# Performance work log

Measured on AMD Instinct MI355X. Metric: run time of the kernel, lower is better.

Reference implementation:

```python
import jax, jax.numpy as jnp
import numpy as np

N_NODES = 50000
N_EDGES = 800000
D = 128
# PNA avg_deg['log'] from deg histogram: all 50000 nodes have degree 16
# avg_deg_log = sum(log(i+1)*deg[i]) / sum(deg) = log(17)
AVG_DEG_LOG = float(np.log(17.0))
EPS = 1e-5  # PyG StdAggregation epsilon


def setup_inputs() -> dict:
    key = jax.random.key(0)
    k1, k2, k3 = jax.random.split(key, 3)
    x = jax.random.normal(k1, (N_EDGES, D), jnp.float32)
    index = jax.random.randint(k2, (N_EDGES,), 0, N_NODES)
    # nn.Linear(12*D, D): weight [out, in]
    W = jax.random.normal(k3, (D, 12 * D), jnp.float32) * 0.02
    b = jnp.zeros((D,), jnp.float32)
    return {"x": x, "index": index, "W": W, "b": b}


def reference(x, index, W, b):
    N = N_NODES
    ones = jnp.ones((x.shape[0],), x.dtype)
    cnt = jax.ops.segment_sum(ones, index, num_segments=N)          # [N] degree
    cnt_c = jnp.maximum(cnt, 1.0)[:, None]                          # clamp(1)
    s1 = jax.ops.segment_sum(x, index, num_segments=N)              # [N, D]
    s2 = jax.ops.segment_sum(x * x, index, num_segments=N)          # [N, D]
    mean = s1 / cnt_c
    var = s2 / cnt_c - mean * mean
    std = jnp.sqrt(jax.nn.relu(var) + EPS)
    mn = jax.ops.segment_min(x, index, num_segments=N)
    mx = jax.ops.segment_max(x, index, num_segments=N)
    empty = (cnt == 0.0)[:, None]
    mn = jnp.where(empty, 0.0, mn)  # torch_scatter fills empty segments with 0
    mx = jnp.where(empty, 0.0, mx)
    agg = jnp.concatenate([mean, mn, mx, std], axis=-1)             # [N, 4D]
    logd = jnp.log(jnp.maximum(cnt, 1.0) + 1.0)[:, None]
    amp = agg * (logd / AVG_DEG_LOG)                                # amplification
    att = agg * (AVG_DEG_LOG / logd)                                # attenuation
    out = jnp.concatenate([agg, amp, att], axis=-1)                 # [N, 12D]
    return out @ W.T + b                                            # [N, D]
```

## Files before the change

kernel.cpp:

```cpp
#include <hip/hip_runtime.h>
#include <hip/hip_bf16.h>

typedef __attribute__((ext_vector_type(8))) __bf16 bf16x8;
typedef __attribute__((ext_vector_type(4))) float f32x4;

#define AVG_DEG_LOG 2.833213344056216f

__device__ __forceinline__ unsigned short f2bf(float f) {
  union { float f; unsigned int u; } a; a.f = f;
  unsigned int r = a.u + 0x7FFFu + ((a.u >> 16) & 1u);
  return (unsigned short)(r >> 16);
}

__global__ void hist_kernel(const int* __restrict__ idx, int* __restrict__ cnt, int E) {
  int i = blockIdx.x * blockDim.x + threadIdx.x;
  if (i < E) atomicAdd(&cnt[idx[i]], 1);
}

__global__ __launch_bounds__(1024) void scan_kernel(const int* __restrict__ cnt,
                                                    int* __restrict__ offsets, int N) {
  __shared__ int partial[1024];
  int t = threadIdx.x;
  int CH = (N + 1023) >> 10;
  int base = t * CH;
  int s = 0;
  for (int i = 0; i < CH; ++i) { int id = base + i; if (id < N) s += cnt[id]; }
  partial[t] = s;
  __syncthreads();
  int val = s;
  for (int off = 1; off < 1024; off <<= 1) {
    int add = (t >= off) ? partial[t - off] : 0;
    __syncthreads();
    val += add;
    partial[t] = val;
    __syncthreads();
  }
  int run = val - s;
  for (int i = 0; i < CH; ++i) {
    int id = base + i;
    if (id < N) { offsets[id] = run; run += cnt[id]; }
  }
  if (t == 1023) offsets[N] = run;
}

__global__ void scatter_kernel(const int* __restrict__ idx, const int* __restrict__ offsets,
                               int* __restrict__ cursor, int* __restrict__ edge_ids, int E) {
  int i = blockIdx.x * blockDim.x + threadIdx.x;
  if (i < E) {
    int n = idx[i];
    int p = atomicAdd(&cursor[n], 1);
    edge_ids[offsets[n] + p] = i;
  }
}

__global__ void wconv_kernel(const float* __restrict__ W, unsigned short* __restrict__ Wb, int n4) {
  int i = blockIdx.x * blockDim.x + threadIdx.x;
  if (i < n4) {
    float4 v = ((const float4*)W)[i];
    ushort4 o;
    o.x = f2bf(v.x); o.y = f2bf(v.y); o.z = f2bf(v.z); o.w = f2bf(v.w);
    ((ushort4*)Wb)[i] = o;
  }
}

__global__ __launch_bounds__(256) void agg_kernel(const float* __restrict__ x,
    const int* __restrict__ edge_ids, const int* __restrict__ offsets,
    unsigned short* __restrict__ agg4, float* __restrict__ amp, float* __restrict__ att, int Nn) {
  int wid = blockIdx.x * 4 + (threadIdx.x >> 6);
  if (wid >= Nn) return;
  int lane = threadIdx.x & 63;
  int offs = offsets[wid];
  int deg = offsets[wid + 1] - offs;
  float s0 = 0.f, s1 = 0.f, q0 = 0.f, q1 = 0.f;
  float mn0 = INFINITY, mn1 = INFINITY, mx0 = -INFINITY, mx1 = -INFINITY;
  int f0 = lane * 2;
  for (int i = 0; i < deg; i += 64) {
    int myid = 0;
    if (i + lane < deg) myid = edge_ids[offs + i + lane];
    int c = deg - i; if (c > 64) c = 64;
    for (int ii = 0; ii < c; ++ii) {
      int e = __shfl(myid, ii, 64);
      float2 v = *(const float2*)(x + (size_t)e * 128 + f0);
      s0 += v.x; s1 += v.y;
      q0 += v.x * v.x; q1 += v.y * v.y;
      mn0 = fminf(mn0, v.x); mn1 = fminf(mn1, v.y);
      mx0 = fmaxf(mx0, v.x); mx1 = fmaxf(mx1, v.y);
    }
  }
  float c = deg > 0 ? (float)deg : 1.0f;
  float inv = 1.0f / c;
  float m0 = s0 * inv, m1 = s1 * inv;
  float v0 = q0 * inv - m0 * m0; v0 = v0 > 0.f ? v0 : 0.f;
  float v1 = q1 * inv - m1 * m1; v1 = v1 > 0.f ? v1 : 0.f;
  float sd0 = sqrtf(v0 + 1e-5f), sd1 = sqrtf(v1 + 1e-5f);
  if (deg == 0) { mn0 = mn1 = mx0 = mx1 = 0.f; }
  size_t rb = (size_t)wid * 512;
  ((unsigned int*)(agg4 + rb      ))[lane] = (unsigned)f2bf(m0)  | ((unsigned)f2bf(m1)  << 16);
  ((unsigned int*)(agg4 + rb + 128))[lane] = (unsigned)f2bf(mn0) | ((unsigned)f2bf(mn1) << 16);
  ((unsigned int*)(agg4 + rb + 256))[lane] = (unsigned)f2bf(mx0) | ((unsigned)f2bf(mx1) << 16);
  ((unsigned int*)(agg4 + rb + 384))[lane] = (unsigned)f2bf(sd0) | ((unsigned)f2bf(sd1) << 16);
  if (lane == 0) {
    float ld = logf(c + 1.0f);
    amp[wid] = ld / AVG_DEG_LOG;
    att[wid] = AVG_DEG_LOG / ld;
  }
}

__global__ __launch_bounds__(256) void gemm_kernel(
    const unsigned short* __restrict__ agg4, const unsigned short* __restrict__ Wb,
    const float* __restrict__ amp, const float* __restrict__ att,
    const float* __restrict__ bias, float* __restrict__ out, int Nn) {
  __shared__ __align__(16) unsigned short As[64][40];
  __shared__ __align__(16) unsigned short Bs[3][128][40];
  __shared__ float ampS[64], attS[64];
  int t = threadIdx.x;
  int m0 = blockIdx.x * 64;
  if (t < 64) {
    int n = m0 + t; if (n > Nn - 1) n = Nn - 1;
    ampS[t] = amp[n]; attS[t] = att[n];
  }
  int wave = t >> 6, lane = t & 63;
  int arow = lane & 15, quad = lane >> 4;
  f32x4 acc[3][8];
#pragma unroll
  for (int g = 0; g < 3; ++g)
#pragma unroll
    for (int c8 = 0; c8 < 8; ++c8) acc[g][c8] = (f32x4){0.f, 0.f, 0.f, 0.f};

  int ar = t >> 2;
  int akc = (t & 3) * 8;
  int agr = m0 + ar; if (agr > Nn - 1) agr = Nn - 1;
  const unsigned short* aptr = agg4 + (size_t)agr * 512 + akc;

  for (int kk = 0; kk < 512; kk += 32) {
    __syncthreads();
    *(uint4*)&As[ar][akc] = *(const uint4*)(aptr + kk);
#pragma unroll
    for (int j = 0; j < 6; ++j) {
      int idx = t + j * 256;
      int g = idx >> 9;
      int rem = idx & 511;
      int n = rem >> 2;
      int kc = (rem & 3) * 8;
      *(uint4*)&Bs[g][n][kc] = *(const uint4*)(Wb + (size_t)n * 1536 + g * 512 + kk + kc);
    }
    __syncthreads();
    bf16x8 af = *(bf16x8*)&As[wave * 16 + arow][quad * 8];
#pragma unroll
    for (int g = 0; g < 3; ++g) {
#pragma unroll
      for (int c8 = 0; c8 < 8; ++c8) {
        bf16x8 bf = *(bf16x8*)&Bs[g][c8 * 16 + arow][quad * 8];
        acc[g][c8] = __builtin_amdgcn_mfma_f32_16x16x32_bf16(af, bf, acc[g][c8], 0, 0, 0);
      }
    }
  }
#pragma unroll
  for (int c8 = 0; c8 < 8; ++c8) {
    int col = c8 * 16 + arow;
    float bv = bias[col];
#pragma unroll
    for (int r = 0; r < 4; ++r) {
      int lrow = wave * 16 + quad * 4 + r;
      int n = m0 + lrow;
      if (n < Nn) {
        float o = acc[0][c8][r] + ampS[lrow] * acc[1][c8][r] + attS[lrow] * acc[2][c8][r] + bv;
        out[(size_t)n * 128 + col] = o;
      }
    }
  }
}

extern "C" void kernel_launch(void* const* d_in, const int* in_sizes, int n_in,
                              void* d_out, int out_size, void* d_ws, size_t ws_size,
                              hipStream_t stream) {
  const float* x     = (const float*)d_in[0];
  const int*   index = (const int*)d_in[1];
  const float* W     = (const float*)d_in[2];
  const float* bias  = (const float*)d_in[3];
  int E  = in_sizes[1];
  int Nn = out_size / 128;
  float* out = (float*)d_out;

  char* ws = (char*)d_ws;
  size_t off = 0;
  int* cnt     = (int*)(ws + off); off += (size_t)Nn * 4;
  int* cursor  = (int*)(ws + off); off += (size_t)Nn * 4;
  int* offsets = (int*)(ws + off); off += (size_t)(Nn + 1) * 4;
  off = (off + 255) & ~(size_t)255;
  int* edge_ids = (int*)(ws + off); off += (size_t)E * 4;
  off = (off + 255) & ~(size_t)255;
  unsigned short* agg4 = (unsigned short*)(ws + off); off += (size_t)Nn * 512 * 2;
  float* amp = (float*)(ws + off); off += (size_t)Nn * 4;
  float* att = (float*)(ws + off); off += (size_t)Nn * 4;
  off = (off + 255) & ~(size_t)255;
  unsigned short* Wb = (unsigned short*)(ws + off); off += (size_t)128 * 1536 * 2;

  hipMemsetAsync(ws, 0, (size_t)Nn * 8, stream);

  int eb = (E + 255) / 256;
  hist_kernel<<<eb, 256, 0, stream>>>(index, cnt, E);
  scan_kernel<<<1, 1024, 0, stream>>>(cnt, offsets, Nn);
  scatter_kernel<<<eb, 256, 0, stream>>>(index, offsets, cursor, edge_ids, E);
  int n4 = 128 * 1536 / 4;
  wconv_kernel<<<(n4 + 255) / 256, 256, 0, stream>>>(W, Wb, n4);
  agg_kernel<<<(Nn + 3) / 4, 256, 0, stream>>>(x, edge_ids, offsets, agg4, amp, att, Nn);
  gemm_kernel<<<(Nn + 63) / 64, 256, 0, stream>>>(agg4, Wb, amp, att, bias, out, Nn);
}
```

Before: 796.6 us.

## Widen agg gathers to float4 with half-wave edge split and fuse hist/wconv

The aggregation kernel now has each half-wave handle a different edge. Each lane loads a 16-byte float4 slice of a row instead of 8 bytes. The gather loop is unrolled to keep four independent non-temporal loads in flight, and the two halves' partials are combined with a cross-half shuffle. The histogram and weight-conversion kernels are merged into one launch to remove a launch. This aims to raise memory-level parallelism on the dominant random-row gather, at the cost of more registers, a remainder path and a final shuffle reduction.

```diff
diff --git a/kernel.cpp b/kernel.cpp
--- a/kernel.cpp
+++ b/kernel.cpp
@@ -12,9 +12,29 @@
   return (unsigned short)(r >> 16);
 }
 
-__global__ void hist_kernel(const int* __restrict__ idx, int* __restrict__ cnt, int E) {
-  int i = blockIdx.x * blockDim.x + threadIdx.x;
-  if (i < E) atomicAdd(&cnt[idx[i]], 1);
+__device__ __forceinline__ uint2 pack4(f32x4 a) {
+  uint2 u;
+  u.x = (unsigned)f2bf(a[0]) | ((unsigned)f2bf(a[1]) << 16);
+  u.y = (unsigned)f2bf(a[2]) | ((unsigned)f2bf(a[3]) << 16);
+  return u;
+}
+
+__global__ void hist_wconv_kernel(const int* __restrict__ idx, int* __restrict__ cnt, int E,
+                                  int hb, const float* __restrict__ W,
+                                  unsigned short* __restrict__ Wb, int n4) {
+  int b = blockIdx.x;
+  if (b < hb) {
+    int i = b * 256 + threadIdx.x;
+    if (i < E) atomicAdd(&cnt[idx[i]], 1);
+  } else {
+    int i = (b - hb) * 256 + threadIdx.x;
+    if (i < n4) {
+      float4 v = ((const float4*)W)[i];
+      ushort4 o;
+      o.x = f2bf(v.x); o.y = f2bf(v.y); o.z = f2bf(v.z); o.w = f2bf(v.w);
+      ((ushort4*)Wb)[i] = o;
+    }
+  }
 }
 
 __global__ __launch_bounds__(1024) void scan_kernel(const int* __restrict__ cnt,
@@ -53,54 +73,86 @@
   }
 }
 
-__global__ void wconv_kernel(const float* __restrict__ W, unsigned short* __restrict__ Wb, int n4) {
-  int i = blockIdx.x * blockDim.x + threadIdx.x;
-  if (i < n4) {
-    float4 v = ((const float4*)W)[i];
-    ushort4 o;
-    o.x = f2bf(v.x); o.y = f2bf(v.y); o.z = f2bf(v.z); o.w = f2bf(v.w);
-    ((ushort4*)Wb)[i] = o;
-  }
-}
-
 __global__ __launch_bounds__(256) void agg_kernel(const float* __restrict__ x,
     const int* __restrict__ edge_ids, const int* __restrict__ offsets,
     unsigned short* __restrict__ agg4, float* __restrict__ amp, float* __restrict__ att, int Nn) {
   int wid = blockIdx.x * 4 + (threadIdx.x >> 6);
   if (wid >= Nn) return;
   int lane = threadIdx.x & 63;
+  int half = lane >> 5;
+  int fh = (lane & 31) * 4;
   int offs = offsets[wid];
   int deg = offsets[wid + 1] - offs;
-  float s0 = 0.f, s1 = 0.f, q0 = 0.f, q1 = 0.f;
-  float mn0 = INFINITY, mn1 = INFINITY, mx0 = -INFINITY, mx1 = -INFINITY;
-  int f0 = lane * 2;
+  f32x4 s = {0.f, 0.f, 0.f, 0.f}, q = {0.f, 0.f, 0.f, 0.f};
+  f32x4 mn = {INFINITY, INFINITY, INFINITY, INFINITY};
+  f32x4 mx = {-INFINITY, -INFINITY, -INFINITY, -INFINITY};
+  const float* xb = x + fh;
   for (int i = 0; i < deg; i += 64) {
     int myid = 0;
     if (i + lane < deg) myid = edge_ids[offs + i + lane];
     int c = deg - i; if (c > 64) c = 64;
-    for (int ii = 0; ii < c; ++ii) {
-      int e = __shfl(myid, ii, 64);
-      float2 v = *(const float2*)(x + (size_t)e * 128 + f0);
-      s0 += v.x; s1 += v.y;
-      q0 += v.x * v.x; q1 += v.y * v.y;
-      mn0 = fminf(mn0, v.x); mn1 = fminf(mn1, v.y);
-      mx0 = fmaxf(mx0, v.x); mx1 = fmaxf(mx1, v.y);
-    }
-  }
-  float c = deg > 0 ? (float)deg : 1.0f;
-  float inv = 1.0f / c;
-  float m0 = s0 * inv, m1 = s1 * inv;
-  float v0 = q0 * inv - m0 * m0; v0 = v0 > 0.f ? v0 : 0.f;
-  float v1 = q1 * inv - m1 * m1; v1 = v1 > 0.f ? v1 : 0.f;
-  float sd0 = sqrtf(v0 + 1e-5f), sd1 = sqrtf(v1 + 1e-5f);
-  if (deg == 0) { mn0 = mn1 = mx0 = mx1 = 0.f; }
+    int ii = 0;
+    for (; ii + 8 <= c; ii += 8) {
+      int e0 = __shfl(myid, ii + half, 64);
+      int e1 = __shfl(myid, ii + 2 + half, 64);
+      int e2 = __shfl(myid, ii + 4 + half, 64);
+      int e3 = __shfl(myid, ii + 6 + half, 64);
+      f32x4 v0 = __builtin_nontemporal_load((const f32x4*)(xb + (size_t)e0 * 128));
+      f32x4 v1 = __builtin_nontemporal_load((const f32x4*)(xb + (size_t)e1 * 128));
+      f32x4 v2 = __builtin_nontemporal_load((const f32x4*)(xb + (size_t)e2 * 128));
+      f32x4 v3 = __builtin_nontemporal_load((const f32x4*)(xb + (size_t)e3 * 128));
+#pragma unroll
+      for (int j = 0; j < 4; ++j) {
+        s[j] += v0[j]; q[j] += v0[j] * v0[j]; mn[j] = fminf(mn[j], v0[j]); mx[j] = fmaxf(mx[j], v0[j]);
+        s[j] += v1[j]; q[j] += v1[j] * v1[j]; mn[j] = fminf(mn[j], v1[j]); mx[j] = fmaxf(mx[j], v1[j]);
+        s[j] += v2[j]; q[j] += v2[j] * v2[j]; mn[j] = fminf(mn[j], v2[j]); mx[j] = fmaxf(mx[j], v2[j]);
+        s[j] += v3[j]; q[j] += v3[j] * v3[j]; mn[j] = fminf(mn[j], v3[j]); mx[j] = fmaxf(mx[j], v3[j]);
+      }
+    }
+    for (; ii < c; ii += 2) {
+      int p = ii + half;
+      bool valid = p < c;
+      int e = __shfl(myid, valid ? p : c - 1, 64);
+      f32x4 v = __builtin_nontemporal_load((const f32x4*)(xb + (size_t)e * 128));
+      if (valid) {
+#pragma unroll
+        for (int j = 0; j < 4; ++j) {
+          s[j] += v[j]; q[j] += v[j] * v[j]; mn[j] = fminf(mn[j], v[j]); mx[j] = fmaxf(mx[j], v[j]);
+        }
+      }
+    }
+  }
+#pragma unroll
+  for (int j = 0; j < 4; ++j) {
+    s[j] += __shfl_xor(s[j], 32, 64);
+    q[j] += __shfl_xor(q[j], 32, 64);
+    mn[j] = fminf(mn[j], __shfl_xor(mn[j], 32, 64));
+    mx[j] = fmaxf(mx[j], __shfl_xor(mx[j], 32, 64));
+  }
+  float cdeg = deg > 0 ? (float)deg : 1.0f;
+  float inv = 1.0f / cdeg;
+  f32x4 mean, sd;
+#pragma unroll
+  for (int j = 0; j < 4; ++j) {
+    mean[j] = s[j] * inv;
+    float var = q[j] * inv - mean[j] * mean[j];
+    var = var > 0.f ? var : 0.f;
+    sd[j] = sqrtf(var + 1e-5f);
+  }
+  if (deg == 0) {
+#pragma unroll
+    for (int j = 0; j < 4; ++j) { mn[j] = 0.f; mx[j] = 0.f; }
+  }
   size_t rb = (size_t)wid * 512;
-  ((unsigned int*)(agg4 + rb      ))[lane] = (unsigned)f2bf(m0)  | ((unsigned)f2bf(m1)  << 16);
-  ((unsigned int*)(agg4 + rb + 128))[lane] = (unsigned)f2bf(mn0) | ((unsigned)f2bf(mn1) << 16);
-  ((unsigned int*)(agg4 + rb + 256))[lane] = (unsigned)f2bf(mx0) | ((unsigned)f2bf(mx1) << 16);
-  ((unsigned int*)(agg4 + rb + 384))[lane] = (unsigned)f2bf(sd0) | ((unsigned)f2bf(sd1) << 16);
+  if (half == 0) {
+    *(uint2*)(agg4 + rb + fh)       = pack4(mean);
+    *(uint2*)(agg4 + rb + 128 + fh) = pack4(mn);
+  } else {
+    *(uint2*)(agg4 + rb + 256 + fh) = pack4(mx);
+    *(uint2*)(agg4 + rb + 384 + fh) = pack4(sd);
+  }
   if (lane == 0) {
-    float ld = logf(c + 1.0f);
+    float ld = logf(cdeg + 1.0f);
     amp[wid] = ld / AVG_DEG_LOG;
     att[wid] = AVG_DEG_LOG / ld;
   }
@@ -199,11 +251,11 @@
   hipMemsetAsync(ws, 0, (size_t)Nn * 8, stream);
 
   int eb = (E + 255) / 256;
-  hist_kernel<<<eb, 256, 0, stream>>>(index, cnt, E);
+  int n4 = 128 * 1536 / 4;
+  int wb = (n4 + 255) / 256;
+  hist_wconv_kernel<<<eb + wb, 256, 0, stream>>>(index, cnt, E, eb, W, Wb, n4);
   scan_kernel<<<1, 1024, 0, stream>>>(cnt, offsets, Nn);
   scatter_kernel<<<eb, 256, 0, stream>>>(index, offsets, cursor, edge_ids, E);
-  int n4 = 128 * 1536 / 4;
-  wconv_kernel<<<(n4 + 255) / 256, 256, 0, stream>>>(W, Wb, n4);
   agg_kernel<<<(Nn + 3) / 4, 256, 0, stream>>>(x, edge_ids, offsets, agg4, amp, att, Nn);
   gemm_kernel<<<(Nn + 63) / 64, 256, 0, stream>>>(agg4, Wb, amp, att, bias, out, Nn);
 }
```

Result: faster. 751.8 us (-5.6%).
